# Optimization experiments

Hardware: AMD Instinct MI355X
Metric: run time of the kernel (lower is better)

The kernel has to match this reference:

```python
import jax, jax.numpy as jnp
import numpy as np

N_BALL = 256
N_EDGES = N_BALL * (N_BALL - 1)  # fully connected, no self loops
BATCH = 4
F_IN = 64
H = 64  # out_channels
EDGE_TYPES = 2


def _edge_structure():
    # receiver repeated pattern / sender covering all other nodes, as in NRI
    recv, send = [], []
    for r in range(N_BALL):
        for s in range(N_BALL):
            if s != r:
                recv.append(r)
                send.append(s)
    eye = np.eye(N_BALL, dtype=np.float32)
    rel_rec = eye[np.array(recv)]   # [E, N]
    rel_send = eye[np.array(send)]  # [E, N]
    return jnp.asarray(rel_rec), jnp.asarray(rel_send)


def setup_inputs() -> dict:
    key = jax.random.key(0)
    ks = jax.random.split(key, 12)
    rel_rec, rel_send = _edge_structure()
    s1 = 1.0 / np.sqrt(2 * F_IN)
    s2 = 1.0 / np.sqrt(H)
    s3 = 1.0 / np.sqrt(F_IN + H)
    return {
        "inputs": jax.random.normal(ks[0], (BATCH, N_BALL, F_IN), jnp.float32),
        "rel_type": jax.random.uniform(ks[1], (BATCH, N_EDGES, EDGE_TYPES), jnp.float32),
        "rel_rec": rel_rec,
        "rel_send": rel_send,
        # per-edge-type message MLPs (stacked over edge types)
        "W1": jax.random.uniform(ks[2], (EDGE_TYPES, 2 * F_IN, H), jnp.float32, -s1, s1),
        "b1": jax.random.uniform(ks[3], (EDGE_TYPES, H), jnp.float32, -s1, s1),
        "W2": jax.random.uniform(ks[4], (EDGE_TYPES, H, H), jnp.float32, -s2, s2),
        "b2": jax.random.uniform(ks[5], (EDGE_TYPES, H), jnp.float32, -s2, s2),
        # output MLP
        "Wo1": jax.random.uniform(ks[6], (F_IN + H, H), jnp.float32, -s3, s3),
        "bo1": jax.random.uniform(ks[7], (H,), jnp.float32, -s3, s3),
        "Wo2": jax.random.uniform(ks[8], (H, H), jnp.float32, -s2, s2),
        "bo2": jax.random.uniform(ks[9], (H,), jnp.float32, -s2, s2),
    }


def reference(inputs, rel_type, rel_rec, rel_send, W1, b1, W2, b2, Wo1, bo1, Wo2, bo2):
    # gather node features onto edges via one-hot matmuls
    receivers = jnp.einsum('en,bnf->bef', rel_rec, inputs)   # [B,E,F]
    senders = jnp.einsum('en,bnf->bef', rel_send, inputs)    # [B,E,F]
    pre_msg = jnp.concatenate([senders, receivers], axis=-1)  # [B,E,2F]

    all_msgs = jnp.zeros(pre_msg.shape[:2] + (H,), dtype=pre_msg.dtype)
    for i in range(EDGE_TYPES):  # skip_first=False -> start at 0
        msg = jax.nn.relu(pre_msg @ W1[i] + b1[i])
        msg = jax.nn.relu(msg @ W2[i] + b2[i])
        all_msgs = all_msgs + msg * rel_type[:, :, i:i + 1]

    # scatter-aggregate edge messages back to receiver nodes
    agg_msgs = jnp.einsum('beh,en->bnh', all_msgs, rel_rec)   # [B,N,H]
    aug_inputs = jnp.concatenate([inputs, agg_msgs], axis=-1)  # [B,N,F+H]

    pred = jax.nn.relu(aug_inputs @ Wo1 + bo1)
    pred = jax.nn.relu(pred @ Wo2 + bo2)
    return inputs + pred
```

## Files before the change

### kernel.cpp

```cpp
#include <hip/hip_runtime.h>
#include <hip/hip_bf16.h>

#define BATCH 4
#define NB    256
#define NE    (NB*(NB-1))

typedef short    short8 __attribute__((ext_vector_type(8)));
typedef float    f32x16 __attribute__((ext_vector_type(16)));

static __device__ __forceinline__ short f2bf(float x) {
    return __builtin_bit_cast(short, __float2bfloat16(x));
}
static __device__ __forceinline__ float bf2f(short s) {
    unsigned u = ((unsigned)(unsigned short)s) << 16;
    return __builtin_bit_cast(float, u);
}
static __device__ __forceinline__ f32x16 splat16(float v) {
    f32x16 r;
    #pragma unroll
    for (int e = 0; e < 16; ++e) r[e] = v;
    return r;
}

#define MFMA(C, A, B) C = __builtin_amdgcn_mfma_f32_32x32x16_bf16(A, B, C, 0, 0, 0)

#define MK_B1(dst, ROW, K0) do {                                               \
    float4 _u0 = *(const float4*)((ROW) + 16*(K0) + 8*lh);                     \
    float4 _u1 = *(const float4*)((ROW) + 16*(K0) + 8*lh + 4);                 \
    short8 _v = { f2bf(_u0.x), f2bf(_u0.y), f2bf(_u0.z), f2bf(_u0.w),          \
                  f2bf(_u1.x), f2bf(_u1.y), f2bf(_u1.z), f2bf(_u1.w) };        \
    (dst) = _v; } while (0)

#define MK_A1(dst, Wp, K0, HT) do {                                            \
    const float* _p = (Wp) + (16*(K0) + 8*lh) * 64 + (l31 + 32*(HT));          \
    short8 _v;                                                                 \
    _v[0]=f2bf(_p[0]);   _v[1]=f2bf(_p[64]);  _v[2]=f2bf(_p[128]);             \
    _v[3]=f2bf(_p[192]); _v[4]=f2bf(_p[256]); _v[5]=f2bf(_p[320]);             \
    _v[6]=f2bf(_p[384]); _v[7]=f2bf(_p[448]);                                  \
    (dst) = _v; } while (0)

__global__ __launch_bounds__(256) void prep_kernel(
    const float* __restrict__ x,
    const float* __restrict__ W1,
    const float* __restrict__ b1,
    const float* __restrict__ W2,
    short* __restrict__ Pbf,
    float* __restrict__ Qg,
    short* __restrict__ W2f)
{
    const int t    = threadIdx.x;
    const int lane = t & 63;
    const int w    = t >> 6;
    const int l31  = lane & 31;
    const int lh   = lane >> 5;
    const int blk  = blockIdx.x;

    if (blk < 8) {
        const int i   = blk >> 2;
        const int b   = blk & 3;
        const int ibb = i * 4 + b;
        const float* xb  = x + (size_t)b * NB * 64;
        const float* w1s = W1 + i * 8192;
        const float* w1r = w1s + 4096;
        const float  b1v0 = b1[i * 64 + l31];
        const float  b1v1 = b1[i * 64 + 32 + l31];

        const float* rowA = xb + (64 * w + l31) * 64;
        const float* rowB = xb + (64 * w + 32 + l31) * 64;
        short8 AR00, AR01, AR02, AR03, AR10, AR11, AR12, AR13;
        MK_B1(AR00, rowA, 0); MK_B1(AR01, rowA, 1);
        MK_B1(AR02, rowA, 2); MK_B1(AR03, rowA, 3);
        MK_B1(AR10, rowB, 0); MK_B1(AR11, rowB, 1);
        MK_B1(AR12, rowB, 2); MK_B1(AR13, rowB, 3);

#define WR_P(C, RT, CT) do {                                                   \
    _Pragma("unroll")                                                          \
    for (int rg = 0; rg < 16; ++rg) {                                          \
        const int nn = 64*w + 32*(RT) + (rg & 3) + 8*(rg >> 2) + 4*lh;         \
        const int hh = l31 + 32*(CT);                                          \
        Pbf[(size_t)ibb*16384 + (hh>>3)*2048 + nn*8 + (hh&7)] = f2bf((C)[rg]); \
    } } while (0)
#define WR_Q0(C, RT, CT) do {                                                  \
    _Pragma("unroll")                                                          \
    for (int rg = 0; rg < 16; ++rg) {                                          \
        const int nn = 64*w + 32*(RT) + (rg & 3) + 8*(rg >> 2) + 4*lh;         \
        Qg[(size_t)ibb*16384 + nn*64 + l31] = (C)[rg] + b1v0;                  \
    } } while (0)
#define WR_Q1(C, RT, CT) do {                                                  \
    _Pragma("unroll")                                                          \
    for (int rg = 0; rg < 16; ++rg) {                                          \
        const int nn = 64*w + 32*(RT) + (rg & 3) + 8*(rg >> 2) + 4*lh;         \
        Qg[(size_t)ibb*16384 + nn*64 + 32 + l31] = (C)[rg] + b1v1;             \
    } } while (0)
#define PREP_GEMM(WSRC, CT, WRM) do {                                          \
    short8 _B0, _B1, _B2, _B3;                                                 \
    MK_A1(_B0, WSRC, 0, CT); MK_A1(_B1, WSRC, 1, CT);                          \
    MK_A1(_B2, WSRC, 2, CT); MK_A1(_B3, WSRC, 3, CT);                          \
    f32x16 _c0 = splat16(0.f), _c1 = splat16(0.f);                             \
    MFMA(_c0, AR00, _B0); MFMA(_c0, AR01, _B1);                                \
    MFMA(_c0, AR02, _B2); MFMA(_c0, AR03, _B3);                                \
    MFMA(_c1, AR10, _B0); MFMA(_c1, AR11, _B1);                                \
    MFMA(_c1, AR12, _B2); MFMA(_c1, AR13, _B3);                                \
    WRM(_c0, 0, CT); WRM(_c1, 1, CT); } while (0)

        PREP_GEMM(w1s, 0, WR_P);
        PREP_GEMM(w1s, 1, WR_P);
        PREP_GEMM(w1r, 0, WR_Q0);
        PREP_GEMM(w1r, 1, WR_Q1);
    } else {
        #pragma unroll
        for (int q = 0; q < 32; ++q) {
            const int e = q * 256 + t;
            const int i = e >> 12, k = (e >> 6) & 63, n = e & 63;
            const float v = W2[e];
            const int k0 = k >> 4, j = k & 7, hm = (k >> 3) & 1;
            const int nt = n >> 5;
            W2f[(((i*2 + nt)*4 + k0)*64 + hm*32 + (n & 31))*8 + j] = f2bf(v);
        }
    }
}


#define MK_A2(dst, PV, I, K0) do {                                             \
    float4 _q0 = *(const float4*)(&qrow[I][16*(K0) + 8*lh]);                   \
    float4 _q1 = *(const float4*)(&qrow[I][16*(K0) + 8*lh + 4]);               \
    short8 _v;                                                                 \
    _v[0] = f2bf(fmaxf(bf2f((PV)[0]) + _q0.x, 0.f));                           \
    _v[1] = f2bf(fmaxf(bf2f((PV)[1]) + _q0.y, 0.f));                           \
    _v[2] = f2bf(fmaxf(bf2f((PV)[2]) + _q0.z, 0.f));                           \
    _v[3] = f2bf(fmaxf(bf2f((PV)[3]) + _q0.w, 0.f));                           \
    _v[4] = f2bf(fmaxf(bf2f((PV)[4]) + _q1.x, 0.f));                           \
    _v[5] = f2bf(fmaxf(bf2f((PV)[5]) + _q1.y, 0.f));                           \
    _v[6] = f2bf(fmaxf(bf2f((PV)[6]) + _q1.z, 0.f));                           \
    _v[7] = f2bf(fmaxf(bf2f((PV)[7]) + _q1.w, 0.f));                           \
    (dst) = _v; } while (0)

#define EPI_QD(C2A, C2B, I, ET, QD) do {                                       \
    float4 _rq = *(const float4*)(&rt2[I][64*w + 32*(ET) + 8*(QD) + 4*lh]);    \
    psum0 += fmaxf((C2A)[4*(QD)],   0.f) * _rq.x;                              \
    psum0 += fmaxf((C2A)[4*(QD)+1], 0.f) * _rq.y;                              \
    psum0 += fmaxf((C2A)[4*(QD)+2], 0.f) * _rq.z;                              \
    psum0 += fmaxf((C2A)[4*(QD)+3], 0.f) * _rq.w;                              \
    psum1 += fmaxf((C2B)[4*(QD)],   0.f) * _rq.x;                              \
    psum1 += fmaxf((C2B)[4*(QD)+1], 0.f) * _rq.y;                              \
    psum1 += fmaxf((C2B)[4*(QD)+2], 0.f) * _rq.z;                              \
    psum1 += fmaxf((C2B)[4*(QD)+3], 0.f) * _rq.w; } while (0)

#define TILE2(I, ET, PA, PB, PC, PD, BVA, BVB) do {                            \
    short8 _a0, _a1, _a2, _a3;                                                 \
    MK_A2(_a0, PA, I, 0); MK_A2(_a1, PB, I, 1);                                \
    MK_A2(_a2, PC, I, 2); MK_A2(_a3, PD, I, 3);                                \
    f32x16 _c2a = splat16(BVA), _c2b = splat16(BVB);                           \
    short8 _w0 = *(const short8*)(W2l + (((I)*8 + 0)*64 + lane)*8);            \
    short8 _w4 = *(const short8*)(W2l + (((I)*8 + 4)*64 + lane)*8);            \
    MFMA(_c2a, _a0, _w0); MFMA(_c2b, _a0, _w4);                                \
    _w0 = *(const short8*)(W2l + (((I)*8 + 1)*64 + lane)*8);                   \
    _w4 = *(const short8*)(W2l + (((I)*8 + 5)*64 + lane)*8);                   \
    MFMA(_c2a, _a1, _w0); MFMA(_c2b, _a1, _w4);                                \
    _w0 = *(const short8*)(W2l + (((I)*8 + 2)*64 + lane)*8);                   \
    _w4 = *(const short8*)(W2l + (((I)*8 + 6)*64 + lane)*8);                   \
    MFMA(_c2a, _a2, _w0); MFMA(_c2b, _a2, _w4);                                \
    _w0 = *(const short8*)(W2l + (((I)*8 + 3)*64 + lane)*8);                   \
    _w4 = *(const short8*)(W2l + (((I)*8 + 7)*64 + lane)*8);                   \
    MFMA(_c2a, _a3, _w0); MFMA(_c2b, _a3, _w4);                                \
    EPI_QD(_c2a, _c2b, I, ET, 0); EPI_QD(_c2a, _c2b, I, ET, 1);                \
    EPI_QD(_c2a, _c2b, I, ET, 2); EPI_QD(_c2a, _c2b, I, ET, 3); } while (0)

#define LD_P(I, K0, S) \
    (*(const short8*)(PbfG + ((size_t)((I)*4+b)*8 + 2*(K0)+lh)*2048 + (size_t)(S)*8))

__global__ __launch_bounds__(256) void main_kernel(
    const float* __restrict__ x,
    const float* __restrict__ rel_type,
    const float* __restrict__ b2,
    const float* __restrict__ Wo1,
    const float* __restrict__ bo1,
    const float* __restrict__ Wo2,
    const float* __restrict__ bo2,
    const short* __restrict__ PbfG,
    const float* __restrict__ Qg,
    const short* __restrict__ W2fG,
    float* __restrict__ out)
{
    const int b    = blockIdx.x >> 8;
    const int r    = blockIdx.x & 255;
    const int t    = threadIdx.x;
    const int lane = t & 63;
    const int w    = t >> 6;
    const int l31  = lane & 31;
    const int lh   = lane >> 5;

    __shared__ __align__(16) short W2l[8192];
    __shared__ __align__(16) float rt2[2][256];
    __shared__ __align__(16) float qrow[2][64];
    __shared__ __align__(16) float red[4][64];
    __shared__ __align__(16) float xl[64];
    __shared__ __align__(16) float aggl[64];
    __shared__ __align__(16) float predl[64];

    const float* xb = x + (size_t)b * NB * 64;

    if (t < 255) {
        const float* p = rel_type + ((size_t)b * NE + (size_t)r * 255 + t) * 2;
        rt2[0][t] = p[0];
        rt2[1][t] = p[1];
    } else {
        rt2[0][255] = 0.f; rt2[1][255] = 0.f;
    }
    #pragma unroll
    for (int q = 0; q < 4; ++q) {
        const int e = (q * 256 + t) * 8;
        *(short8*)(W2l + e) = *(const short8*)(W2fG + e);
    }
    if (t < 128) {
        const int i = t >> 6, h = t & 63;
        qrow[i][h] = Qg[(size_t)(i * 4 + b) * 16384 + r * 64 + h];
    }
    if (t >= 192) xl[t - 192] = xb[r * 64 + (t - 192)];

    const int kap0 = 64 * w + l31;
    const int kap1 = kap0 + 32;
    int s0 = (kap0 < r) ? kap0 : kap0 + 1; if (s0 > 255) s0 = 255;
    int s1 = (kap1 < r) ? kap1 : kap1 + 1; if (s1 > 255) s1 = 255;

    short8 P000 = LD_P(0,0,s0), P001 = LD_P(0,1,s0), P002 = LD_P(0,2,s0), P003 = LD_P(0,3,s0);
    short8 P010 = LD_P(0,0,s1), P011 = LD_P(0,1,s1), P012 = LD_P(0,2,s1), P013 = LD_P(0,3,s1);
    short8 P100 = LD_P(1,0,s0), P101 = LD_P(1,1,s0), P102 = LD_P(1,2,s0), P103 = LD_P(1,3,s0);
    short8 P110 = LD_P(1,0,s1), P111 = LD_P(1,1,s1), P112 = LD_P(1,2,s1), P113 = LD_P(1,3,s1);

    const float bv00 = b2[l31],      bv01 = b2[32 + l31];
    const float bv10 = b2[64 + l31], bv11 = b2[96 + l31];

    __syncthreads();

    float psum0 = 0.f, psum1 = 0.f;

    TILE2(0, 0, P000, P001, P002, P003, bv00, bv01);
    TILE2(0, 1, P010, P011, P012, P013, bv00, bv01);
    TILE2(1, 0, P100, P101, P102, P103, bv10, bv11);
    TILE2(1, 1, P110, P111, P112, P113, bv10, bv11);

    psum0 += __shfl_xor(psum0, 32, 64);
    psum1 += __shfl_xor(psum1, 32, 64);
    if (lh == 0) {
        red[w][l31]      = psum0;
        red[w][l31 + 32] = psum1;
    }
    __syncthreads();
    if (t < 64) aggl[t] = red[0][t] + red[1][t] + red[2][t] + red[3][t];
    __syncthreads();

    {
        const float* src = (w < 2) ? (xl + w * 32) : (aggl + (w - 2) * 32);
        const float* Wp  = Wo1 + (w * 32) * 64 + lane;
        float s = 0.f;
        #pragma unroll
        for (int jj = 0; jj < 32; ++jj) s = fmaf(src[jj], Wp[jj * 64], s);
        red[w][lane] = s;
    }
    __syncthreads();
    if (t < 64)
        predl[t] = fmaxf(red[0][t] + red[1][t] + red[2][t] + red[3][t] + bo1[t], 0.f);
    __syncthreads();

    {
        const float* Wp = Wo2 + (w * 16) * 64 + lane;
        float s = 0.f;
        #pragma unroll
        for (int jj = 0; jj < 16; ++jj) s = fmaf(predl[w * 16 + jj], Wp[jj * 64], s);
        red[w][lane] = s;
    }
    __syncthreads();
    if (t < 64)
        out[((size_t)b * NB + r) * 64 + t] =
            xl[t] + fmaxf(red[0][t] + red[1][t] + red[2][t] + red[3][t] + bo2[t], 0.f);
}

extern "C" void kernel_launch(void* const* d_in, const int* in_sizes, int n_in,
                              void* d_out, int out_size, void* d_ws, size_t ws_size,
                              hipStream_t stream) {
    (void)in_sizes; (void)n_in; (void)out_size; (void)ws_size;

    const float* x    = (const float*)d_in[0];
    const float* rt   = (const float*)d_in[1];
    const float* W1   = (const float*)d_in[4];
    const float* b1   = (const float*)d_in[5];
    const float* W2   = (const float*)d_in[6];
    const float* b2   = (const float*)d_in[7];
    const float* Wo1  = (const float*)d_in[8];
    const float* bo1  = (const float*)d_in[9];
    const float* Wo2  = (const float*)d_in[10];
    const float* bo2  = (const float*)d_in[11];
    float* out = (float*)d_out;

    char* ws = (char*)d_ws;
    short* Pbf = (short*)ws;
    float* Qg  = (float*)(ws + 262144);
    short* W2f = (short*)(ws + 786432);

    prep_kernel<<<9, 256, 0, stream>>>(x, W1, b1, W2, Pbf, Qg, W2f);
    main_kernel<<<BATCH * NB, 256, 0, stream>>>(x, rt, b2, Wo1, bo1, Wo2, bo2,
                                                Pbf, Qg, W2f, out);
}
```

Baseline: 25.09 us.

## Split prep GEMM across more blocks via LDS staging, cut main-kernel register pressure

The prep kernel now uses 16 GEMM blocks, each handling half the nodes. Each block stages W1 in fp32 and x in swizzled bf16 in shared memory, so operand fragments come from LDS instead of strided global loads. The main kernel defers loading the second edge type's P fragments until after the first type's tiles, builds A operands one at a time in TILE2, and adds a launch bound of 4 blocks per CU to lower register use and raise occupancy. rel_type is read as a float2. The risks are extra LDS in prep and possible spills or exposed load latency from the tighter register budget.

```diff
diff --git a/kernel.cpp b/kernel.cpp
--- a/kernel.cpp
+++ b/kernel.cpp
@@ -24,15 +24,8 @@
 
 #define MFMA(C, A, B) C = __builtin_amdgcn_mfma_f32_32x32x16_bf16(A, B, C, 0, 0, 0)
 
-#define MK_B1(dst, ROW, K0) do {                                               \
-    float4 _u0 = *(const float4*)((ROW) + 16*(K0) + 8*lh);                     \
-    float4 _u1 = *(const float4*)((ROW) + 16*(K0) + 8*lh + 4);                 \
-    short8 _v = { f2bf(_u0.x), f2bf(_u0.y), f2bf(_u0.z), f2bf(_u0.w),          \
-                  f2bf(_u1.x), f2bf(_u1.y), f2bf(_u1.z), f2bf(_u1.w) };        \
-    (dst) = _v; } while (0)
-
-#define MK_A1(dst, Wp, K0, HT) do {                                            \
-    const float* _p = (Wp) + (16*(K0) + 8*lh) * 64 + (l31 + 32*(HT));          \
+#define MK_BW(dst, BASE, K0, NT) do {                                          \
+    const float* _p = W1l + (BASE) + (16*(K0) + 8*lh) * 64 + l31 + 32*(NT);    \
     short8 _v;                                                                 \
     _v[0]=f2bf(_p[0]);   _v[1]=f2bf(_p[64]);  _v[2]=f2bf(_p[128]);             \
     _v[3]=f2bf(_p[192]); _v[4]=f2bf(_p[256]); _v[5]=f2bf(_p[320]);             \
@@ -55,58 +48,94 @@
     const int lh   = lane >> 5;
     const int blk  = blockIdx.x;
 
-    if (blk < 8) {
-        const int i   = blk >> 2;
-        const int b   = blk & 3;
-        const int ibb = i * 4 + b;
-        const float* xb  = x + (size_t)b * NB * 64;
-        const float* w1s = W1 + i * 8192;
-        const float* w1r = w1s + 4096;
-        const float  b1v0 = b1[i * 64 + l31];
-        const float  b1v1 = b1[i * 64 + 32 + l31];
-
-        const float* rowA = xb + (64 * w + l31) * 64;
-        const float* rowB = xb + (64 * w + 32 + l31) * 64;
-        short8 AR00, AR01, AR02, AR03, AR10, AR11, AR12, AR13;
-        MK_B1(AR00, rowA, 0); MK_B1(AR01, rowA, 1);
-        MK_B1(AR02, rowA, 2); MK_B1(AR03, rowA, 3);
-        MK_B1(AR10, rowB, 0); MK_B1(AR11, rowB, 1);
-        MK_B1(AR12, rowB, 2); MK_B1(AR13, rowB, 3);
-
-#define WR_P(C, RT, CT) do {                                                   \
-    _Pragma("unroll")                                                          \
-    for (int rg = 0; rg < 16; ++rg) {                                          \
-        const int nn = 64*w + 32*(RT) + (rg & 3) + 8*(rg >> 2) + 4*lh;         \
-        const int hh = l31 + 32*(CT);                                          \
-        Pbf[(size_t)ibb*16384 + (hh>>3)*2048 + nn*8 + (hh&7)] = f2bf((C)[rg]); \
-    } } while (0)
-#define WR_Q0(C, RT, CT) do {                                                  \
-    _Pragma("unroll")                                                          \
-    for (int rg = 0; rg < 16; ++rg) {                                          \
-        const int nn = 64*w + 32*(RT) + (rg & 3) + 8*(rg >> 2) + 4*lh;         \
-        Qg[(size_t)ibb*16384 + nn*64 + l31] = (C)[rg] + b1v0;                  \
-    } } while (0)
-#define WR_Q1(C, RT, CT) do {                                                  \
-    _Pragma("unroll")                                                          \
-    for (int rg = 0; rg < 16; ++rg) {                                          \
-        const int nn = 64*w + 32*(RT) + (rg & 3) + 8*(rg >> 2) + 4*lh;         \
-        Qg[(size_t)ibb*16384 + nn*64 + 32 + l31] = (C)[rg] + b1v1;             \
-    } } while (0)
-#define PREP_GEMM(WSRC, CT, WRM) do {                                          \
-    short8 _B0, _B1, _B2, _B3;                                                 \
-    MK_A1(_B0, WSRC, 0, CT); MK_A1(_B1, WSRC, 1, CT);                          \
-    MK_A1(_B2, WSRC, 2, CT); MK_A1(_B3, WSRC, 3, CT);                          \
-    f32x16 _c0 = splat16(0.f), _c1 = splat16(0.f);                             \
-    MFMA(_c0, AR00, _B0); MFMA(_c0, AR01, _B1);                                \
-    MFMA(_c0, AR02, _B2); MFMA(_c0, AR03, _B3);                                \
-    MFMA(_c1, AR10, _B0); MFMA(_c1, AR11, _B1);                                \
-    MFMA(_c1, AR12, _B2); MFMA(_c1, AR13, _B3);                                \
-    WRM(_c0, 0, CT); WRM(_c1, 1, CT); } while (0)
-
-        PREP_GEMM(w1s, 0, WR_P);
-        PREP_GEMM(w1s, 1, WR_P);
-        PREP_GEMM(w1r, 0, WR_Q0);
-        PREP_GEMM(w1r, 1, WR_Q1);
+    __shared__ __align__(16) float W1l[8192];
+    __shared__ __align__(16) short xbf[8192];
+
+    if (blk < 16) {
+        const int i    = blk >> 3;
+        const int b    = (blk >> 1) & 3;
+        const int half = blk & 1;
+        const int n0   = half * 128;
+        const int ibb  = i * 4 + b;
+        const float* xb = x + (size_t)b * NB * 64;
+
+        #pragma unroll
+        for (int q = 0; q < 8; ++q) {
+            const int e = (q * 256 + t) * 4;
+            *(float4*)(W1l + e) = *(const float4*)(W1 + (size_t)i * 8192 + e);
+        }
+        #pragma unroll
+        for (int rep = 0; rep < 2; ++rep) {
+            const int n  = (t >> 2) + 64 * rep;
+            const int f0 = (t & 3) * 16;
+            const float* src = xb + (n0 + n) * 64 + f0;
+            float4 v0 = *(const float4*)(src);
+            float4 v1 = *(const float4*)(src + 4);
+            float4 v2 = *(const float4*)(src + 8);
+            float4 v3 = *(const float4*)(src + 12);
+            short8 s0 = { f2bf(v0.x), f2bf(v0.y), f2bf(v0.z), f2bf(v0.w),
+                          f2bf(v1.x), f2bf(v1.y), f2bf(v1.z), f2bf(v1.w) };
+            short8 s1 = { f2bf(v2.x), f2bf(v2.y), f2bf(v2.z), f2bf(v2.w),
+                          f2bf(v3.x), f2bf(v3.y), f2bf(v3.z), f2bf(v3.w) };
+            const int sw = (n & 7) << 4;
+            *(short8*)((char*)xbf + n * 128 + ((f0 * 2)      ^ sw)) = s0;
+            *(short8*)((char*)xbf + n * 128 + ((f0 * 2 + 16) ^ sw)) = s1;
+        }
+        __syncthreads();
+
+        const int rloc = 32 * w + l31;
+        const int swr  = (rloc & 7) << 4;
+        const short8 XB0 = *(const short8*)((const char*)xbf + rloc*128 + ((16*lh)       ^ swr));
+        const short8 XB1 = *(const short8*)((const char*)xbf + rloc*128 + ((32 + 16*lh)  ^ swr));
+        const short8 XB2 = *(const short8*)((const char*)xbf + rloc*128 + ((64 + 16*lh)  ^ swr));
+        const short8 XB3 = *(const short8*)((const char*)xbf + rloc*128 + ((96 + 16*lh)  ^ swr));
+
+        {
+            short8 B0, B1, B2, B3;
+            MK_BW(B0, 0, 0, 0); MK_BW(B1, 0, 1, 0); MK_BW(B2, 0, 2, 0); MK_BW(B3, 0, 3, 0);
+            f32x16 c = splat16(0.f);
+            MFMA(c, XB0, B0); MFMA(c, XB1, B1); MFMA(c, XB2, B2); MFMA(c, XB3, B3);
+            #pragma unroll
+            for (int rg = 0; rg < 16; ++rg) {
+                const int nn = n0 + 32*w + (rg & 3) + 8*(rg >> 2) + 4*lh;
+                Pbf[(size_t)ibb*16384 + (l31 >> 3)*2048 + nn*8 + (l31 & 7)] = f2bf(c[rg]);
+            }
+        }
+        {
+            short8 B0, B1, B2, B3;
+            MK_BW(B0, 0, 0, 1); MK_BW(B1, 0, 1, 1); MK_BW(B2, 0, 2, 1); MK_BW(B3, 0, 3, 1);
+            f32x16 c = splat16(0.f);
+            MFMA(c, XB0, B0); MFMA(c, XB1, B1); MFMA(c, XB2, B2); MFMA(c, XB3, B3);
+            #pragma unroll
+            for (int rg = 0; rg < 16; ++rg) {
+                const int nn = n0 + 32*w + (rg & 3) + 8*(rg >> 2) + 4*lh;
+                Pbf[(size_t)ibb*16384 + (4 + (l31 >> 3))*2048 + nn*8 + (l31 & 7)] = f2bf(c[rg]);
+            }
+        }
+        {
+            short8 B0, B1, B2, B3;
+            MK_BW(B0, 4096, 0, 0); MK_BW(B1, 4096, 1, 0); MK_BW(B2, 4096, 2, 0); MK_BW(B3, 4096, 3, 0);
+            f32x16 c = splat16(0.f);
+            MFMA(c, XB0, B0); MFMA(c, XB1, B1); MFMA(c, XB2, B2); MFMA(c, XB3, B3);
+            const float b1v = b1[i * 64 + l31];
+            #pragma unroll
+            for (int rg = 0; rg < 16; ++rg) {
+                const int nn = n0 + 32*w + (rg & 3) + 8*(rg >> 2) + 4*lh;
+                Qg[(size_t)ibb*16384 + nn*64 + l31] = c[rg] + b1v;
+            }
+        }
+        {
+            short8 B0, B1, B2, B3;
+            MK_BW(B0, 4096, 0, 1); MK_BW(B1, 4096, 1, 1); MK_BW(B2, 4096, 2, 1); MK_BW(B3, 4096, 3, 1);
+            f32x16 c = splat16(0.f);
+            MFMA(c, XB0, B0); MFMA(c, XB1, B1); MFMA(c, XB2, B2); MFMA(c, XB3, B3);
+            const float b1v = b1[i * 64 + 32 + l31];
+            #pragma unroll
+            for (int rg = 0; rg < 16; ++rg) {
+                const int nn = n0 + 32*w + (rg & 3) + 8*(rg >> 2) + 4*lh;
+                Qg[(size_t)ibb*16384 + nn*64 + 32 + l31] = c[rg] + b1v;
+            }
+        }
     } else {
         #pragma unroll
         for (int q = 0; q < 32; ++q) {
@@ -147,29 +176,31 @@
     psum1 += fmaxf((C2B)[4*(QD)+3], 0.f) * _rq.w; } while (0)
 
 #define TILE2(I, ET, PA, PB, PC, PD, BVA, BVB) do {                            \
-    short8 _a0, _a1, _a2, _a3;                                                 \
-    MK_A2(_a0, PA, I, 0); MK_A2(_a1, PB, I, 1);                                \
-    MK_A2(_a2, PC, I, 2); MK_A2(_a3, PD, I, 3);                                \
     f32x16 _c2a = splat16(BVA), _c2b = splat16(BVB);                           \
-    short8 _w0 = *(const short8*)(W2l + (((I)*8 + 0)*64 + lane)*8);            \
-    short8 _w4 = *(const short8*)(W2l + (((I)*8 + 4)*64 + lane)*8);            \
-    MFMA(_c2a, _a0, _w0); MFMA(_c2b, _a0, _w4);                                \
+    short8 _a, _w0, _w4;                                                       \
+    MK_A2(_a, PA, I, 0);                                                       \
+    _w0 = *(const short8*)(W2l + (((I)*8 + 0)*64 + lane)*8);                   \
+    _w4 = *(const short8*)(W2l + (((I)*8 + 4)*64 + lane)*8);                   \
+    MFMA(_c2a, _a, _w0); MFMA(_c2b, _a, _w4);                                  \
+    MK_A2(_a, PB, I, 1);                                                       \
     _w0 = *(const short8*)(W2l + (((I)*8 + 1)*64 + lane)*8);                   \
     _w4 = *(const short8*)(W2l + (((I)*8 + 5)*64 + lane)*8);                   \
-    MFMA(_c2a, _a1, _w0); MFMA(_c2b, _a1, _w4);                                \
+    MFMA(_c2a, _a, _w0); MFMA(_c2b, _a, _w4);                                  \
+    MK_A2(_a, PC, I, 2);                                                       \
     _w0 = *(const short8*)(W2l + (((I)*8 + 2)*64 + lane)*8);                   \
     _w4 = *(const short8*)(W2l + (((I)*8 + 6)*64 + lane)*8);                   \
-    MFMA(_c2a, _a2, _w0); MFMA(_c2b, _a2, _w4);                                \
+    MFMA(_c2a, _a, _w0); MFMA(_c2b, _a, _w4);                                  \
+    MK_A2(_a, PD, I, 3);                                                       \
     _w0 = *(const short8*)(W2l + (((I)*8 + 3)*64 + lane)*8);                   \
     _w4 = *(const short8*)(W2l + (((I)*8 + 7)*64 + lane)*8);                   \
-    MFMA(_c2a, _a3, _w0); MFMA(_c2b, _a3, _w4);                                \
+    MFMA(_c2a, _a, _w0); MFMA(_c2b, _a, _w4);                                  \
     EPI_QD(_c2a, _c2b, I, ET, 0); EPI_QD(_c2a, _c2b, I, ET, 1);                \
     EPI_QD(_c2a, _c2b, I, ET, 2); EPI_QD(_c2a, _c2b, I, ET, 3); } while (0)
 
 #define LD_P(I, K0, S) \
     (*(const short8*)(PbfG + ((size_t)((I)*4+b)*8 + 2*(K0)+lh)*2048 + (size_t)(S)*8))
 
-__global__ __launch_bounds__(256) void main_kernel(
+__global__ __launch_bounds__(256, 4) void main_kernel(
     const float* __restrict__ x,
     const float* __restrict__ rel_type,
     const float* __restrict__ b2,
@@ -201,9 +232,9 @@
     const float* xb = x + (size_t)b * NB * 64;
 
     if (t < 255) {
-        const float* p = rel_type + ((size_t)b * NE + (size_t)r * 255 + t) * 2;
-        rt2[0][t] = p[0];
-        rt2[1][t] = p[1];
+        const float2 pv = *(const float2*)(rel_type + ((size_t)b * NE + (size_t)r * 255 + t) * 2);
+        rt2[0][t] = pv.x;
+        rt2[1][t] = pv.y;
     } else {
         rt2[0][255] = 0.f; rt2[1][255] = 0.f;
     }
@@ -225,8 +256,6 @@
 
     short8 P000 = LD_P(0,0,s0), P001 = LD_P(0,1,s0), P002 = LD_P(0,2,s0), P003 = LD_P(0,3,s0);
     short8 P010 = LD_P(0,0,s1), P011 = LD_P(0,1,s1), P012 = LD_P(0,2,s1), P013 = LD_P(0,3,s1);
-    short8 P100 = LD_P(1,0,s0), P101 = LD_P(1,1,s0), P102 = LD_P(1,2,s0), P103 = LD_P(1,3,s0);
-    short8 P110 = LD_P(1,0,s1), P111 = LD_P(1,1,s1), P112 = LD_P(1,2,s1), P113 = LD_P(1,3,s1);
 
     const float bv00 = b2[l31],      bv01 = b2[32 + l31];
     const float bv10 = b2[64 + l31], bv11 = b2[96 + l31];
@@ -237,8 +266,13 @@
 
     TILE2(0, 0, P000, P001, P002, P003, bv00, bv01);
     TILE2(0, 1, P010, P011, P012, P013, bv00, bv01);
-    TILE2(1, 0, P100, P101, P102, P103, bv10, bv11);
-    TILE2(1, 1, P110, P111, P112, P113, bv10, bv11);
+
+    {
+        short8 Q000 = LD_P(1,0,s0), Q001 = LD_P(1,1,s0), Q002 = LD_P(1,2,s0), Q003 = LD_P(1,3,s0);
+        short8 Q010 = LD_P(1,0,s1), Q011 = LD_P(1,1,s1), Q012 = LD_P(1,2,s1), Q013 = LD_P(1,3,s1);
+        TILE2(1, 0, Q000, Q001, Q002, Q003, bv10, bv11);
+        TILE2(1, 1, Q010, Q011, Q012, Q013, bv10, bv11);
+    }
 
     psum0 += __shfl_xor(psum0, 32, 64);
     psum1 += __shfl_xor(psum1, 32, 64);
@@ -298,7 +332,7 @@
     float* Qg  = (float*)(ws + 262144);
     short* W2f = (short*)(ws + 786432);
 
-    prep_kernel<<<9, 256, 0, stream>>>(x, W1, b1, W2, Pbf, Qg, W2f);
+    prep_kernel<<<17, 256, 0, stream>>>(x, W1, b1, W2, Pbf, Qg, W2f);
     main_kernel<<<BATCH * NB, 256, 0, stream>>>(x, rt, b2, Wo1, bo1, Wo2, bo2,
                                                 Pbf, Qg, W2f, out);
 }
```

Result: slower. 49.17 us (+96.0%).
